# Kernel optimization log

Measured on AMD Instinct MI355X. Metric: run time of the kernel, lower is better.

The kernel has to match this reference:

```python
import jax, jax.numpy as jnp
import numpy as np

N = 50000      # num_nodes
E = 800000     # num_edges
D = 128        # hidden_dim
POOL_RATIO = 0.5
CROSS_W = 1.0  # cross_weight


def _gcn(x, W, b, src, dst, n):
    """GCNConv: symmetric-normalized aggregation with self-loops. Dropout is identity (eval)."""
    loops = jnp.arange(n)
    s = jnp.concatenate([src, loops])
    d = jnp.concatenate([dst, loops])
    deg = jax.ops.segment_sum(jnp.ones(s.shape, x.dtype), d, num_segments=n)
    inv_sqrt = jax.lax.rsqrt(jnp.maximum(deg, 1.0))  # deg >= 1 due to self-loops
    xw = x @ W                                        # [n, D]
    msg = xw[s] * (inv_sqrt[s] * inv_sqrt[d])[:, None]  # [E+n, D] gather
    return jax.ops.segment_sum(msg, d, num_segments=n) + b


def _prelu(x, a):
    return jnp.where(x >= 0, x, a * x)


def setup_inputs() -> dict:
    key = jax.random.key(0)
    ks = jax.random.split(key, 8)
    glorot = lambda k, sh: jax.random.normal(k, sh, jnp.float32) * np.float32(np.sqrt(2.0 / (sh[0] + sh[1])))
    return {
        "feat": jax.random.normal(ks[0], (N, D), jnp.float32),
        "h_neg": jax.random.normal(ks[1], (N, D), jnp.float32),
        "edge_index": jax.random.randint(ks[2], (2, E), 0, N),
        "Wd": glorot(ks[3], (D, D)),
        "bd": jnp.zeros((D,), jnp.float32),
        "prelu_a": jnp.full((1,), 0.25, jnp.float32),
        "Wbil": glorot(ks[4], (D, D)),
        "bbil": jnp.zeros((1,), jnp.float32),
        "Wg1": glorot(ks[5], (D, D)),
        "bg1": jnp.zeros((D,), jnp.float32),
        "Wg2": glorot(ks[6], (D, D)),
        "bg2": jnp.zeros((D,), jnp.float32),
        "Wg3": glorot(ks[7], (D, D)),
        "bg3": jnp.zeros((D,), jnp.float32),
    }


def reference(feat, h_neg, edge_index, Wd, bd, prelu_a, Wbil, bbil,
              Wg1, bg1, Wg2, bg2, Wg3, bg3):
    src, dst = edge_index[0], edge_index[1]
    # --- IndexSelect: dense layer on pos/neg features ---
    h_pos = _prelu(feat @ Wd + bd, prelu_a)
    h_neg_d = _prelu(h_neg @ Wd + bd, prelu_a)
    embed = _gcn(h_pos, Wg1, bg1, src, dst, N)
    h_center = jax.nn.sigmoid(embed)
    # Discriminator (bilinear) positive scores -> node importance
    score_pos = jnp.einsum('nd,de,ne->n', h_pos, Wbil, h_center) + bbil[0]
    _ = jnp.einsum('nd,de,ne->n', h_neg_d, Wbil, h_center) + bbil[0]  # score_neg (logits branch)
    scores = jax.nn.sigmoid(score_pos)
    order = jnp.argsort(-scores)           # descending
    k = int(POOL_RATIO * N)
    select_idx = order[:k]
    select_scores = scores[order][:k]
    # --- GraphPool (use_gcn=True): down-sample GCN, gather, scale ---
    pooled = _gcn(embed, Wg2, bg2, src, dst, N)[select_idx] * select_scores[:, None]
    # --- GraphUnpool: scatter into zeros, up-sample GCN ---
    fine = jnp.zeros((N, D), feat.dtype).at[select_idx].set(pooled)
    out = _gcn(fine, Wg3, bg3, src, dst, N)
    # --- cross/fuse connection ---
    return out + CROSS_W * embed
```

## Files before the change

### kernel.cpp

```cpp
#include <hip/hip_runtime.h>
#include <hip/hip_bf16.h>

#define NN 50000
#define NE 800000
#define DD 128
#define KSEL 25000
#define NBK 391
#define NBLKA 98

typedef unsigned int uint32;
typedef unsigned short ushort16;

__device__ __forceinline__ float sigmoidf(float x){ return 1.f/(1.f+__expf(-x)); }

__device__ __forceinline__ unsigned short f2b(float f){
  union{float f; unsigned u;} v; v.f=f;
  unsigned r=(v.u + 0x7fffu + ((v.u>>16)&1u))>>16;
  return (unsigned short)r;
}

__device__ __forceinline__ void addbf2(float&lo,float&hi,uint32 u,float w){
  lo+=__uint_as_float(u<<16)*w;
  hi+=__uint_as_float(u&0xffff0000u)*w;
}

__global__ __launch_bounds__(1024) void k_bcount(const int* __restrict__ dst,
    int* __restrict__ btot, int* __restrict__ blkcnt){
  __shared__ int h[NBK];
  int tid=threadIdx.x;
  for(int i=tid;i<NBK;i+=1024) h[i]=0;
  __syncthreads();
  int e0=blockIdx.x*8192;
  #pragma unroll
  for(int t=0;t<8;t++){
    int e=e0+t*1024+tid;
    if(e<NE) atomicAdd(&h[dst[e]>>7],1);
  }
  __syncthreads();
  for(int i=tid;i<NBK;i+=1024){
    int c=h[i];
    blkcnt[blockIdx.x*NBK+i]=c;
    if(c) atomicAdd(&btot[i],c);
  }
}

__global__ __launch_bounds__(512) void k_bscan(const int* __restrict__ btot,
    int* __restrict__ boff, const int* __restrict__ blkcnt, int* __restrict__ blkbase,
    int* __restrict__ row_start){
  __shared__ int sdata[512];
  int tid=threadIdx.x;
  int v=(tid<NBK)?btot[tid]:0;
  sdata[tid]=v; __syncthreads();
  for(int off=1;off<512;off<<=1){
    int y=(tid>=off)?sdata[tid-off]:0;
    __syncthreads();
    sdata[tid]+=y;
    __syncthreads();
  }
  int excl=sdata[tid]-v;
  if(tid<NBK) boff[tid]=excl;
  if(tid==NBK-1){ boff[NBK]=excl+v; row_start[NN]=NE; }
  if(tid<NBK){
    int run=excl;
    for(int b=0;b<NBLKA;b++){
      int c=blkcnt[b*NBK+tid];
      blkbase[b*NBK+tid]=run;
      run+=c;
    }
  }
}

__global__ __launch_bounds__(1024) void k_bscatter(const int* __restrict__ src,
    const int* __restrict__ dst, const int* __restrict__ blkbase, uint32* __restrict__ pairs){
  __shared__ int cur[NBK];
  int tid=threadIdx.x;
  for(int i=tid;i<NBK;i+=1024) cur[i]=blkbase[blockIdx.x*NBK+i];
  __syncthreads();
  int e0=blockIdx.x*8192;
  #pragma unroll
  for(int t=0;t<8;t++){
    int e=e0+t*1024+tid;
    if(e<NE){
      int d=dst[e];
      int p=atomicAdd(&cur[d>>7],1);
      pairs[p]=(unsigned)src[e] | ((unsigned)(d&127)<<17);
    }
  }
}

__global__ __launch_bounds__(256) void k_bfinal(const uint32* __restrict__ pairs,
    const int* __restrict__ boff, int* __restrict__ row_start,
    float* __restrict__ inv_sq, int* __restrict__ csr_src){
  __shared__ int degl[128];
  __shared__ int cur[128];
  __shared__ int ssum[2];
  int b=blockIdx.x, tid=threadIdx.x;
  int lo=boff[b], hi=boff[b+1];
  if(tid<128) degl[tid]=0;
  __syncthreads();
  for(int e=lo+tid;e<hi;e+=256) atomicAdd(&degl[pairs[e]>>17],1);
  __syncthreads();
  int v=0,x=0;
  if(tid<128){
    v=degl[tid]; x=v;
    #pragma unroll
    for(int off=1;off<64;off<<=1){
      int y=__shfl_up(x,off,64);
      if((tid&63)>=off) x+=y;
    }
    if((tid&63)==63) ssum[tid>>6]=x;
  }
  __syncthreads();
  if(tid<128){
    int incl=x+((tid>=64)?ssum[0]:0);
    int node=b*128+tid;
    int excl=lo+incl-v;
    if(node<NN){
      row_start[node]=excl;
      cur[tid]=excl;
      inv_sq[node]=1.f/sqrtf((float)(v+1));
    }
  }
  __syncthreads();
  for(int e=lo+tid;e<hi;e+=256){
    uint32 u=pairs[e];
    int p=atomicAdd(&cur[u>>17],1);
    csr_src[p]=(int)(u&0x1FFFFu);
  }
}

__global__ void k_transpose(const float* __restrict__ W, float* __restrict__ Wt){
  int idx=blockIdx.x*256+threadIdx.x;
  if(idx<DD*DD){
    int k=idx>>7, c=idx&127;
    Wt[idx]=W[c*DD+k];
  }
}

template<int IN_SIG,int ACT,int OUT_BF16,int FUSE_SCORE>
__global__ __launch_bounds__(256) void k_gemm96(const float* __restrict__ A,
    const float* __restrict__ W, const float* __restrict__ bias,
    float* __restrict__ outf, ushort16* __restrict__ outb,
    const float* __restrict__ aparam, const float* __restrict__ hp,
    const float* __restrict__ bbil, float* __restrict__ score){
  __shared__ float Al[96][132];
  int tid=threadIdx.x;
  int row0=blockIdx.x*96;
  {
    const float4* A4=(const float4*)(A+(size_t)row0*DD);
    #pragma unroll
    for(int i=0;i<12;i++){
      int idx=i*256+tid;
      int r=idx>>5, c=(idx&31)*4;
      float4 v=make_float4(0.f,0.f,0.f,0.f);
      if(row0+r<NN) v=A4[idx];
      if(IN_SIG){ v.x=sigmoidf(v.x); v.y=sigmoidf(v.y); v.z=sigmoidf(v.z); v.w=sigmoidf(v.w); }
      *(float4*)&Al[r][c]=v;
    }
  }
  __syncthreads();
  int tx=tid&15, ty=tid>>4;
  float acc[6][8];
  #pragma unroll
  for(int i=0;i<6;i++)
    #pragma unroll
    for(int c=0;c<8;c++) acc[i][c]=0.f;

  for(int k=0;k<DD;k+=4){
    float wv[4][8];
    #pragma unroll
    for(int r=0;r<4;r++){
      float4 lo=*(const float4*)&W[(size_t)(k+r)*DD+tx*8];
      float4 hi=*(const float4*)&W[(size_t)(k+r)*DD+tx*8+4];
      wv[r][0]=lo.x; wv[r][1]=lo.y; wv[r][2]=lo.z; wv[r][3]=lo.w;
      wv[r][4]=hi.x; wv[r][5]=hi.y; wv[r][6]=hi.z; wv[r][7]=hi.w;
    }
    #pragma unroll
    for(int i=0;i<6;i++){
      float4 a=*(const float4*)&Al[ty+16*i][k];
      #pragma unroll
      for(int c=0;c<8;c++)
        acc[i][c]+=a.x*wv[0][c]+a.y*wv[1][c]+a.z*wv[2][c]+a.w*wv[3][c];
    }
  }

  if(FUSE_SCORE){
    float bb=bbil[0];
    #pragma unroll
    for(int i=0;i<6;i++){
      int r=row0+ty+16*i;
      float p=0.f;
      if(r<NN){
        float4 h0=*(const float4*)&hp[(size_t)r*DD+tx*8];
        float4 h1=*(const float4*)&hp[(size_t)r*DD+tx*8+4];
        p=acc[i][0]*h0.x+acc[i][1]*h0.y+acc[i][2]*h0.z+acc[i][3]*h0.w
         +acc[i][4]*h1.x+acc[i][5]*h1.y+acc[i][6]*h1.z+acc[i][7]*h1.w;
      }
      p+=__shfl_xor(p,1,64); p+=__shfl_xor(p,2,64);
      p+=__shfl_xor(p,4,64); p+=__shfl_xor(p,8,64);
      if(tx==0 && r<NN) score[r]=sigmoidf(p+bb);
    }
    return;
  }
  float bl[8]={0,0,0,0,0,0,0,0};
  if(bias){
    float4 b0=*(const float4*)&bias[tx*8];
    float4 b1=*(const float4*)&bias[tx*8+4];
    bl[0]=b0.x; bl[1]=b0.y; bl[2]=b0.z; bl[3]=b0.w;
    bl[4]=b1.x; bl[5]=b1.y; bl[6]=b1.z; bl[7]=b1.w;
  }
  float ap=ACT?aparam[0]:0.f;
  #pragma unroll
  for(int i=0;i<6;i++){
    int r=row0+ty+16*i;
    if(r<NN){
      float o[8];
      #pragma unroll
      for(int c=0;c<8;c++){
        float t=acc[i][c]+bl[c];
        if(ACT) t=t>=0.f?t:ap*t;
        o[c]=t;
      }
      if(OUT_BF16){
        uint4 pk;
        pk.x=((uint32)f2b(o[1])<<16)|f2b(o[0]);
        pk.y=((uint32)f2b(o[3])<<16)|f2b(o[2]);
        pk.z=((uint32)f2b(o[5])<<16)|f2b(o[4]);
        pk.w=((uint32)f2b(o[7])<<16)|f2b(o[6]);
        *(uint4*)&outb[(size_t)r*DD+tx*8]=pk;
      } else {
        float4 q0; q0.x=o[0]; q0.y=o[1]; q0.z=o[2]; q0.w=o[3];
        float4 q1; q1.x=o[4]; q1.y=o[5]; q1.z=o[6]; q1.w=o[7];
        *(float4*)&outf[(size_t)r*DD+tx*8]=q0;
        *(float4*)&outf[(size_t)r*DD+tx*8+4]=q1;
      }
    }
  }
}

__global__ __launch_bounds__(256) void k_agg_f32(const float* __restrict__ xw,
    const int* __restrict__ row_start, const int* __restrict__ csr,
    const float* __restrict__ inv, const float* __restrict__ bias,
    float* __restrict__ outp){
  int node=blockIdx.x*4+(threadIdx.x>>6);
  if(node>=NN) return;
  int lane=threadIdx.x&63;
  int g=lane>>5, li=lane&31;
  int rs=row_start[node], re=row_start[node+1];
  float a0=0.f,a1=0.f,a2=0.f,a3=0.f;
  int j=rs;
  for(; j+7<re; j+=8){
    int s0=csr[j+g], s1=csr[j+2+g], s2=csr[j+4+g], s3=csr[j+6+g];
    float w0=inv[s0], w1=inv[s1], w2=inv[s2], w3=inv[s3];
    float4 v0=*(const float4*)&xw[(size_t)s0*DD+li*4];
    float4 v1=*(const float4*)&xw[(size_t)s1*DD+li*4];
    float4 v2=*(const float4*)&xw[(size_t)s2*DD+li*4];
    float4 v3=*(const float4*)&xw[(size_t)s3*DD+li*4];
    a0+=v0.x*w0+v1.x*w1+v2.x*w2+v3.x*w3;
    a1+=v0.y*w0+v1.y*w1+v2.y*w2+v3.y*w3;
    a2+=v0.z*w0+v1.z*w1+v2.z*w2+v3.z*w3;
    a3+=v0.w*w0+v1.w*w1+v2.w*w2+v3.w*w3;
  }
  for(; j+1<re; j+=2){
    int s=csr[j+g];
    float w=inv[s];
    float4 v=*(const float4*)&xw[(size_t)s*DD+li*4];
    a0+=v.x*w; a1+=v.y*w; a2+=v.z*w; a3+=v.w*w;
  }
  if(j<re && g==0){
    int s=csr[j]; float w=inv[s];
    float4 v=*(const float4*)&xw[(size_t)s*DD+li*4];
    a0+=v.x*w; a1+=v.y*w; a2+=v.z*w; a3+=v.w*w;
  }
  if(g==0){
    float wd=inv[node];
    float4 v=*(const float4*)&xw[(size_t)node*DD+li*4];
    a0+=v.x*wd; a1+=v.y*wd; a2+=v.z*wd; a3+=v.w*wd;
  }
  a0+=__shfl_xor(a0,32,64); a1+=__shfl_xor(a1,32,64);
  a2+=__shfl_xor(a2,32,64); a3+=__shfl_xor(a3,32,64);
  if(g==0){
    float wn=inv[node];
    float4 bv=*(const float4*)&bias[li*4];
    float4 o;
    o.x=a0*wn+bv.x; o.y=a1*wn+bv.y; o.z=a2*wn+bv.z; o.w=a3*wn+bv.w;
    *(float4*)&outp[(size_t)node*DD+li*4]=o;
  }
}

template<int MODE>
__global__ __launch_bounds__(256) void k_agg_b16(const uint32* __restrict__ xwb,
    const int* __restrict__ row_start, const int* __restrict__ csr,
    const float* __restrict__ inv, const float* __restrict__ bias,
    float* __restrict__ outp, const float* __restrict__ score,
    const unsigned char* __restrict__ sel, const float* __restrict__ addbuf){
  int node=blockIdx.x*4+(threadIdx.x>>6);
  if(node>=NN) return;
  int lane=threadIdx.x&63;
  if(MODE==1 && !sel[node]){
    float2 z; z.x=0.f; z.y=0.f;
    *(float2*)&outp[(size_t)node*DD+lane*2]=z;
    return;
  }
  int g=lane>>4, li=lane&15;
  int rs=row_start[node], re=row_start[node+1];
  float a[8];
  #pragma unroll
  for(int c=0;c<8;c++) a[c]=0.f;
  int j=rs;
  for(; j+7<re; j+=8){
    int sA=csr[j+g], sB=csr[j+4+g];
    if(MODE!=2 || sel[sA]){
      float w=inv[sA];
      uint4 u=*(const uint4*)(xwb+(size_t)sA*64+li*4);
      addbf2(a[0],a[1],u.x,w); addbf2(a[2],a[3],u.y,w);
      addbf2(a[4],a[5],u.z,w); addbf2(a[6],a[7],u.w,w);
    }
    if(MODE!=2 || sel[sB]){
      float w=inv[sB];
      uint4 u=*(const uint4*)(xwb+(size_t)sB*64+li*4);
      addbf2(a[0],a[1],u.x,w); addbf2(a[2],a[3],u.y,w);
      addbf2(a[4],a[5],u.z,w); addbf2(a[6],a[7],u.w,w);
    }
  }
  for(; j+3<re; j+=4){
    int s=csr[j+g];
    if(MODE!=2 || sel[s]){
      float w=inv[s];
      uint4 u=*(const uint4*)(xwb+(size_t)s*64+li*4);
      addbf2(a[0],a[1],u.x,w); addbf2(a[2],a[3],u.y,w);
      addbf2(a[4],a[5],u.z,w); addbf2(a[6],a[7],u.w,w);
    }
  }
  int rem=re-j;
  if(g<rem){
    int s=csr[j+g];
    if(MODE!=2 || sel[s]){
      float w=inv[s];
      uint4 u=*(const uint4*)(xwb+(size_t)s*64+li*4);
      addbf2(a[0],a[1],u.x,w); addbf2(a[2],a[3],u.y,w);
      addbf2(a[4],a[5],u.z,w); addbf2(a[6],a[7],u.w,w);
    }
  }
  if(g==0 && (MODE!=2 || sel[node])){
    float wd=inv[node];
    uint4 u=*(const uint4*)(xwb+(size_t)node*64+li*4);
    addbf2(a[0],a[1],u.x,wd); addbf2(a[2],a[3],u.y,wd);
    addbf2(a[4],a[5],u.z,wd); addbf2(a[6],a[7],u.w,wd);
  }
  #pragma unroll
  for(int c=0;c<8;c++){
    a[c]+=__shfl_xor(a[c],16,64);
    a[c]+=__shfl_xor(a[c],32,64);
  }
  if(g<2){
    float wn=inv[node];
    int cb=li*8+g*4;
    float4 bv=*(const float4*)&bias[cb];
    float r0=a[g*4+0]*wn+bv.x, r1=a[g*4+1]*wn+bv.y;
    float r2=a[g*4+2]*wn+bv.z, r3=a[g*4+3]*wn+bv.w;
    if(MODE==1){
      float sc=score[node];
      r0*=sc; r1*=sc; r2*=sc; r3*=sc;
    } else {
      float4 ad=*(const float4*)&addbuf[(size_t)node*DD+cb];
      r0+=ad.x; r1+=ad.y; r2+=ad.z; r3+=ad.w;
    }
    float4 o; o.x=r0; o.y=r1; o.z=r2; o.w=r3;
    *(float4*)&outp[(size_t)node*DD+cb]=o;
  }
}

template<int NB,int PASS>
__global__ __launch_bounds__(256) void k_hist(const float* __restrict__ score,
    int* __restrict__ ghist, const int* __restrict__ ctrl){
  __shared__ int lh[NB];
  int tid=threadIdx.x;
  for(int i=tid;i<NB;i+=256) lh[i]=0;
  __syncthreads();
  int p0=0,p01=0;
  if(PASS==1) p0=ctrl[0];
  if(PASS==2) p01=ctrl[2];
  for(int i=blockIdx.x*256+tid; i<NN; i+=gridDim.x*256){
    unsigned b=__float_as_uint(score[i]);
    if(PASS==0) atomicAdd(&lh[b>>20],1);
    else if(PASS==1){ if((int)(b>>20)==p0) atomicAdd(&lh[(b>>8)&0xFFF],1); }
    else { if((int)(b>>8)==p01) atomicAdd(&lh[b&0xFF],1); }
  }
  __syncthreads();
  for(int i=tid;i<NB;i+=256){ int v=lh[i]; if(v) atomicAdd(&ghist[i],v); }
}

template<int NB,int PASS>
__global__ void k_findb(const int* __restrict__ hist, int* __restrict__ ctrl){
  const int NT=NB/4;
  __shared__ int gsum[NT];
  int t=threadIdx.x;
  int s=hist[t*4]+hist[t*4+1]+hist[t*4+2]+hist[t*4+3];
  int x=s; gsum[t]=x; __syncthreads();
  for(int off=1;off<NT;off<<=1){
    int y=(t+off<NT)?gsum[t+off]:0;
    __syncthreads();
    x+=y; gsum[t]=x; __syncthreads();
  }
  int base;
  if(PASS==0) base=0; else if(PASS==1) base=ctrl[1]; else base=ctrl[3];
  int above=base+((t<NT-1)?gsum[t+1]:0);
  int incl=base+gsum[t];
  if(above<KSEL && incl>=KSEL){
    int c=above, B=0;
    for(int b=3;b>=0;b--){
      int hb=hist[t*4+b];
      if(c+hb>=KSEL){ B=t*4+b; break; }
      c+=hb;
    }
    if(PASS==0){ ctrl[0]=B; ctrl[1]=c; }
    else if(PASS==1){ ctrl[2]=(ctrl[0]<<12)|B; ctrl[3]=c; }
    else { ctrl[4]=(int)((((unsigned)ctrl[2])<<8)|(unsigned)B); ctrl[5]=KSEL-c; }
  }
}

__global__ void k_sel(const float* __restrict__ score, int* __restrict__ ctrl,
                      int* __restrict__ tie_list, unsigned char* __restrict__ sel){
  int i=blockIdx.x*256+threadIdx.x;
  if(i>=NN) return;
  unsigned b=__float_as_uint(score[i]);
  unsigned thr=(unsigned)ctrl[4];
  if(b>thr){ sel[i]=1; }
  else if(b==thr){
    sel[i]=0;
    int p=atomicAdd(&ctrl[6],1);
    if(p<4096) tie_list[p]=i;
  } else sel[i]=0;
}

__global__ __launch_bounds__(256) void k_tie(const int* __restrict__ ctrl,
    const int* __restrict__ tie_list, unsigned char* __restrict__ sel){
  int m=ctrl[6]; if(m>4096) m=4096;
  int needed=ctrl[5];
  for(int t=threadIdx.x; t<m; t+=blockDim.x){
    int idx=tie_list[t];
    int rank=0;
    for(int j=0;j<m;j++) rank+=(tie_list[j]<idx)?1:0;
    if(rank<needed) sel[idx]=1;
  }
}

extern "C" void kernel_launch(void* const* d_in, const int* in_sizes, int n_in,
                              void* d_out, int out_size, void* d_ws, size_t ws_size,
                              hipStream_t stream){
  const float* feat   =(const float*)d_in[0];
  const int*   ei     =(const int*)  d_in[2];
  const int*   src    = ei;
  const int*   dst    = ei + NE;
  const float* Wd     =(const float*)d_in[3];
  const float* bd     =(const float*)d_in[4];
  const float* prelu_a=(const float*)d_in[5];
  const float* Wbil   =(const float*)d_in[6];
  const float* bbil   =(const float*)d_in[7];
  const float* Wg1    =(const float*)d_in[8];
  const float* bg1    =(const float*)d_in[9];
  const float* Wg2    =(const float*)d_in[10];
  const float* bg2    =(const float*)d_in[11];
  const float* Wg3    =(const float*)d_in[12];
  const float* bg3    =(const float*)d_in[13];
  float* out=(float*)d_out;

  char* p=(char*)d_ws;
  auto alloc=[&](size_t bytes)->void*{ void* r=(void*)p; p+=((bytes+255)/256)*256; return r; };
  float* h_pos   =(float*)alloc((size_t)NN*DD*4);
  float* embed   =(float*)alloc((size_t)NN*DD*4);
  float* xw      =(float*)alloc((size_t)NN*DD*4);
  float* score   =(float*)alloc((size_t)NN*4);
  float* inv_sq  =(float*)alloc((size_t)NN*4);
  float* WbT     =(float*)alloc((size_t)DD*DD*4);
  int*   row_st  =(int*)  alloc((size_t)(NN+1)*4);
  int*   csr_src =(int*)  alloc((size_t)NE*4);
  int*   ctrl    =(int*)  alloc(64);
  int*   hist0   =(int*)  alloc(4096*4);
  int*   hist1   =(int*)  alloc(4096*4);
  int*   hist2   =(int*)  alloc(256*4);
  int*   tie_list=(int*)  alloc(4096*4);
  unsigned char* sel=(unsigned char*)alloc(NN);
  int*   btot    =(int*)  alloc((size_t)NBK*4);
  int*   boff    =(int*)  alloc((size_t)(NBK+1)*4);
  int*   blkcnt  =(int*)  alloc((size_t)NBLKA*NBK*4);
  int*   blkbase =(int*)  alloc((size_t)NBLKA*NBK*4);
  uint32* pairs  =(uint32*)xw;
  ushort16* xwb  =(ushort16*)xw;
  float* fine = out;

  const int NB=(NN+255)/256;
  const int GB=(NN+95)/96;
  const int AB=(NN+3)/4;

  hipMemsetAsync(ctrl, 0, (size_t)((char*)tie_list-(char*)ctrl), stream);
  hipMemsetAsync(btot, 0, (size_t)NBK*4, stream);

  k_bcount  <<<NBLKA,1024,0,stream>>>(dst, btot, blkcnt);
  k_bscan   <<<1,512,0,stream>>>(btot, boff, blkcnt, blkbase, row_st);
  k_bscatter<<<NBLKA,1024,0,stream>>>(src, dst, blkbase, pairs);
  k_bfinal  <<<NBK,256,0,stream>>>(pairs, boff, row_st, inv_sq, csr_src);
  k_transpose<<<64,256,0,stream>>>(Wbil, WbT);

  k_gemm96<0,1,0,0><<<GB,256,0,stream>>>(feat, Wd, bd, h_pos, nullptr, prelu_a, nullptr, nullptr, nullptr);
  k_gemm96<0,0,0,0><<<GB,256,0,stream>>>(h_pos, Wg1, nullptr, xw, nullptr, nullptr, nullptr, nullptr, nullptr);
  k_agg_f32<<<AB,256,0,stream>>>(xw, row_st, csr_src, inv_sq, bg1, embed);
  k_gemm96<1,0,0,1><<<GB,256,0,stream>>>(embed, WbT, nullptr, nullptr, nullptr, nullptr, h_pos, bbil, score);
  k_hist<4096,0><<<64,256,0,stream>>>(score, hist0, ctrl);
  k_findb<4096,0><<<1,1024,0,stream>>>(hist0, ctrl);
  k_hist<4096,1><<<64,256,0,stream>>>(score, hist1, ctrl);
  k_findb<4096,1><<<1,1024,0,stream>>>(hist1, ctrl);
  k_hist<256,2><<<64,256,0,stream>>>(score, hist2, ctrl);
  k_findb<256,2><<<1,64,0,stream>>>(hist2, ctrl);
  k_sel<<<NB,256,0,stream>>>(score, ctrl, tie_list, sel);
  k_tie<<<1,256,0,stream>>>(ctrl, tie_list, sel);
  k_gemm96<0,0,1,0><<<GB,256,0,stream>>>(embed, Wg2, nullptr, nullptr, xwb, nullptr, nullptr, nullptr, nullptr);
  k_agg_b16<1><<<AB,256,0,stream>>>((const uint32*)xwb, row_st, csr_src, inv_sq, bg2, fine, score, sel, nullptr);
  k_gemm96<0,0,1,0><<<GB,256,0,stream>>>(fine, Wg3, nullptr, nullptr, xwb, nullptr, nullptr, nullptr, nullptr);
  k_agg_b16<2><<<AB,256,0,stream>>>((const uint32*)xwb, row_st, csr_src, inv_sq, bg3, out, nullptr, sel, embed);
}
```

Baseline: 371.7 us.

## Compact selected nodes into a list and restrict pool aggregation and GEMM to them

The selection and tie-break kernels now append each selected node index to a compact list through an atomic counter. The pooled aggregation then launches only over the KSEL listed nodes, instead of over all nodes with early zero writes for the unselected ones. The up-sample GEMM gathers its input rows through the same list, so only selected rows of the scattered buffer are multiplied. Unselected rows of that buffer are never written or read, which relies on the final aggregation still skipping unselected sources via the sel mask. The list order is nondeterministic because of the atomics, which adds scattered row loads and stores in the GEMM.

Measured after the change: 374.4 us. Within noise of the previous version (+0.7%).

```diff
diff --git a/kernel.cpp b/kernel.cpp
--- a/kernel.cpp
+++ b/kernel.cpp
@@ -137,23 +137,26 @@
   }
 }
 
-template<int IN_SIG,int ACT,int OUT_BF16,int FUSE_SCORE>
+template<int IN_SIG,int ACT,int OUT_BF16,int FUSE_SCORE,int ROWLIST>
 __global__ __launch_bounds__(256) void k_gemm96(const float* __restrict__ A,
     const float* __restrict__ W, const float* __restrict__ bias,
     float* __restrict__ outf, ushort16* __restrict__ outb,
     const float* __restrict__ aparam, const float* __restrict__ hp,
-    const float* __restrict__ bbil, float* __restrict__ score){
+    const float* __restrict__ bbil, float* __restrict__ score,
+    const int* __restrict__ rlist){
   __shared__ float Al[96][132];
   int tid=threadIdx.x;
   int row0=blockIdx.x*96;
   {
-    const float4* A4=(const float4*)(A+(size_t)row0*DD);
     #pragma unroll
     for(int i=0;i<12;i++){
       int idx=i*256+tid;
       int r=idx>>5, c=(idx&31)*4;
+      int gr; bool ok;
+      if(ROWLIST){ int ri=row0+r; ok=(ri<KSEL); gr=ok?rlist[ri]:0; }
+      else { gr=row0+r; ok=(gr<NN); }
       float4 v=make_float4(0.f,0.f,0.f,0.f);
-      if(row0+r<NN) v=A4[idx];
+      if(ok) v=*(const float4*)&A[(size_t)gr*DD+c];
       if(IN_SIG){ v.x=sigmoidf(v.x); v.y=sigmoidf(v.y); v.z=sigmoidf(v.z); v.w=sigmoidf(v.w); }
       *(float4*)&Al[r][c]=v;
     }
@@ -212,8 +215,11 @@
   float ap=ACT?aparam[0]:0.f;
   #pragma unroll
   for(int i=0;i<6;i++){
-    int r=row0+ty+16*i;
-    if(r<NN){
+    int ri=row0+ty+16*i;
+    int r; bool ok;
+    if(ROWLIST){ ok=(ri<KSEL); r=ok?rlist[ri]:0; }
+    else { r=ri; ok=(r<NN); }
+    if(ok){
       float o[8];
       #pragma unroll
       for(int c=0;c<8;c++){
@@ -293,15 +299,13 @@
     const int* __restrict__ row_start, const int* __restrict__ csr,
     const float* __restrict__ inv, const float* __restrict__ bias,
     float* __restrict__ outp, const float* __restrict__ score,
-    const unsigned char* __restrict__ sel, const float* __restrict__ addbuf){
-  int node=blockIdx.x*4+(threadIdx.x>>6);
-  if(node>=NN) return;
+    const unsigned char* __restrict__ sel, const float* __restrict__ addbuf,
+    const int* __restrict__ list){
+  int idx4=blockIdx.x*4+(threadIdx.x>>6);
+  int node;
+  if(MODE==1){ if(idx4>=KSEL) return; node=list[idx4]; }
+  else { node=idx4; if(node>=NN) return; }
   int lane=threadIdx.x&63;
-  if(MODE==1 && !sel[node]){
-    float2 z; z.x=0.f; z.y=0.f;
-    *(float2*)&outp[(size_t)node*DD+lane*2]=z;
-    return;
-  }
   int g=lane>>4, li=lane&15;
   int rs=row_start[node], re=row_start[node+1];
   float a[8];
@@ -421,12 +425,17 @@
 }
 
 __global__ void k_sel(const float* __restrict__ score, int* __restrict__ ctrl,
-                      int* __restrict__ tie_list, unsigned char* __restrict__ sel){
+                      int* __restrict__ tie_list, unsigned char* __restrict__ sel,
+                      int* __restrict__ list){
   int i=blockIdx.x*256+threadIdx.x;
   if(i>=NN) return;
   unsigned b=__float_as_uint(score[i]);
   unsigned thr=(unsigned)ctrl[4];
-  if(b>thr){ sel[i]=1; }
+  if(b>thr){
+    sel[i]=1;
+    int p=atomicAdd(&ctrl[7],1);
+    list[p]=i;
+  }
   else if(b==thr){
     sel[i]=0;
     int p=atomicAdd(&ctrl[6],1);
@@ -434,15 +443,20 @@
   } else sel[i]=0;
 }
 
-__global__ __launch_bounds__(256) void k_tie(const int* __restrict__ ctrl,
-    const int* __restrict__ tie_list, unsigned char* __restrict__ sel){
-  int m=ctrl[6]; if(m>4096) m=4096;
-  int needed=ctrl[5];
+__global__ __launch_bounds__(256) void k_tie(const int* __restrict__ ctrl_c,
+    int* __restrict__ ctrl, const int* __restrict__ tie_list,
+    unsigned char* __restrict__ sel, int* __restrict__ list){
+  int m=ctrl_c[6]; if(m>4096) m=4096;
+  int needed=ctrl_c[5];
   for(int t=threadIdx.x; t<m; t+=blockDim.x){
     int idx=tie_list[t];
     int rank=0;
     for(int j=0;j<m;j++) rank+=(tie_list[j]<idx)?1:0;
-    if(rank<needed) sel[idx]=1;
+    if(rank<needed){
+      sel[idx]=1;
+      int p=atomicAdd(&ctrl[7],1);
+      list[p]=idx;
+    }
   }
 }
 
@@ -481,6 +495,7 @@
   int*   hist1   =(int*)  alloc(4096*4);
   int*   hist2   =(int*)  alloc(256*4);
   int*   tie_list=(int*)  alloc(4096*4);
+  int*   list    =(int*)  alloc((size_t)KSEL*4);
   unsigned char* sel=(unsigned char*)alloc(NN);
   int*   btot    =(int*)  alloc((size_t)NBK*4);
   int*   boff    =(int*)  alloc((size_t)(NBK+1)*4);
@@ -492,7 +507,9 @@
 
   const int NB=(NN+255)/256;
   const int GB=(NN+95)/96;
+  const int GBL=(KSEL+95)/96;
   const int AB=(NN+3)/4;
+  const int ABL=(KSEL+3)/4;
 
   hipMemsetAsync(ctrl, 0, (size_t)((char*)tie_list-(char*)ctrl), stream);
   hipMemsetAsync(btot, 0, (size_t)NBK*4, stream);
@@ -503,20 +520,20 @@
   k_bfinal  <<<NBK,256,0,stream>>>(pairs, boff, row_st, inv_sq, csr_src);
   k_transpose<<<64,256,0,stream>>>(Wbil, WbT);
 
-  k_gemm96<0,1,0,0><<<GB,256,0,stream>>>(feat, Wd, bd, h_pos, nullptr, prelu_a, nullptr, nullptr, nullptr);
-  k_gemm96<0,0,0,0><<<GB,256,0,stream>>>(h_pos, Wg1, nullptr, xw, nullptr, nullptr, nullptr, nullptr, nullptr);
+  k_gemm96<0,1,0,0,0><<<GB,256,0,stream>>>(feat, Wd, bd, h_pos, nullptr, prelu_a, nullptr, nullptr, nullptr, nullptr);
+  k_gemm96<0,0,0,0,0><<<GB,256,0,stream>>>(h_pos, Wg1, nullptr, xw, nullptr, nullptr, nullptr, nullptr, nullptr, nullptr);
   k_agg_f32<<<AB,256,0,stream>>>(xw, row_st, csr_src, inv_sq, bg1, embed);
-  k_gemm96<1,0,0,1><<<GB,256,0,stream>>>(embed, WbT, nullptr, nullptr, nullptr, nullptr, h_pos, bbil, score);
+  k_gemm96<1,0,0,1,0><<<GB,256,0,stream>>>(embed, WbT, nullptr, nullptr, nullptr, nullptr, h_pos, bbil, score, nullptr);
   k_hist<4096,0><<<64,256,0,stream>>>(score, hist0, ctrl);
   k_findb<4096,0><<<1,1024,0,stream>>>(hist0, ctrl);
   k_hist<4096,1><<<64,256,0,stream>>>(score, hist1, ctrl);
   k_findb<4096,1><<<1,1024,0,stream>>>(hist1, ctrl);
   k_hist<256,2><<<64,256,0,stream>>>(score, hist2, ctrl);
   k_findb<256,2><<<1,64,0,stream>>>(hist2, ctrl);
-  k_sel<<<NB,256,0,stream>>>(score, ctrl, tie_list, sel);
-  k_tie<<<1,256,0,stream>>>(ctrl, tie_list, sel);
-  k_gemm96<0,0,1,0><<<GB,256,0,stream>>>(embed, Wg2, nullptr, nullptr, xwb, nullptr, nullptr, nullptr, nullptr);
-  k_agg_b16<1><<<AB,256,0,stream>>>((const uint32*)xwb, row_st, csr_src, inv_sq, bg2, fine, score, sel, nullptr);
-  k_gemm96<0,0,1,0><<<GB,256,0,stream>>>(fine, Wg3, nullptr, nullptr, xwb, nullptr, nullptr, nullptr, nullptr);
-  k_agg_b16<2><<<AB,256,0,stream>>>((const uint32*)xwb, row_st, csr_src, inv_sq, bg3, out, nullptr, sel, embed);
-}
+  k_sel<<<NB,256,0,stream>>>(score, ctrl, tie_list, sel, list);
+  k_tie<<<1,256,0,stream>>>(ctrl, ctrl, tie_list, sel, list);
+  k_gemm96<0,0,1,0,0><<<GB,256,0,stream>>>(embed, Wg2, nullptr, nullptr, xwb, nullptr, nullptr, nullptr, nullptr, nullptr);
+  k_agg_b16<1><<<ABL,256,0,stream>>>((const uint32*)xwb, row_st, csr_src, inv_sq, bg2, fine, score, sel, nullptr, list);
+  k_gemm96<0,0,1,0,1><<<GBL,256,0,stream>>>(fine, Wg3, nullptr, nullptr, xwb, nullptr, nullptr, nullptr, nullptr, list);
+  k_agg_b16<2><<<AB,256,0,stream>>>((const uint32*)xwb, row_st, csr_src, inv_sq, bg3, out, nullptr, sel, embed, nullptr);
+}
```
